# Performance work log

Hardware: AMD Instinct MI355X
Metric: run time of the kernel (lower is better)

Reference implementation:

```python
import jax, jax.numpy as jnp
import numpy as np

LOG_HALF = float(np.log(0.5))  # log_g(0) = log(relu(0)+0.5) = log(0.5)

def log_g(x):
    # log of g(x) = where(x>=0, x+0.5, sigmoid(x))
    return jnp.where(x >= 0.0, jnp.log(jnp.maximum(x, 0.0) + 0.5), -jax.nn.softplus(-x))

def setup_inputs() -> dict:
    key = jax.random.key(0)
    k1, k2, k3, k4 = jax.random.split(key, 4)
    B, T, D, E = 4, 4096, 1024, 1536
    x = jax.random.normal(k1, (B, T, D), dtype=jnp.float32)
    W_f = jax.random.normal(k2, (2 * E, D), dtype=jnp.float32) * 0.02
    b_f = jax.random.normal(k3, (2 * E,), dtype=jnp.float32) * 0.02
    W_down = jax.random.normal(k4, (D, E), dtype=jnp.float32) * 0.02
    return {"x": x, "W_f": W_f, "b_f": b_f, "W_down": W_down}

def reference(x, W_f, b_f, W_down):
    B, T, D = x.shape
    E = W_down.shape[1]
    # fused input projection, split into gate pre-act k and candidate pre-act h_x
    kz, h_x = jnp.split(jnp.einsum('btd,ed->bte', x, W_f) + b_f, 2, axis=-1)
    log_z = -jax.nn.softplus(-kz)          # log sigmoid(k)
    log_coeffs = -jax.nn.softplus(kz)      # log (1 - sigmoid(k))
    log_tilde_h = log_g(h_x)
    # prepend initial log hidden state log_g(0) = log 0.5
    log_h0 = jnp.full((B, 1, E), LOG_HALF, dtype=x.dtype)
    log_values = jnp.concatenate([log_h0, log_tilde_h + log_z], axis=1)  # (B, T+1, E)
    # a_star = pad(cumsum(log_coeffs), one zero row at front along time)
    a_star = jnp.concatenate(
        [jnp.zeros((B, 1, E), dtype=x.dtype), jnp.cumsum(log_coeffs, axis=1)], axis=1)
    log_h = a_star + jax.lax.cumlogsumexp(log_values - a_star, axis=1)
    h = jnp.exp(log_h)[:, 1:]              # (B, T, E)
    return jnp.einsum('bte,de->btd', h, W_down)
```

## Files before the change

### kernel.cpp

```cpp
#include <hip/hip_runtime.h>
#include <hip/hip_bf16.h>
#include <stdint.h>


typedef __bf16 bf16x8 __attribute__((ext_vector_type(8)));
typedef float  f32x4  __attribute__((ext_vector_type(4)));

__device__ __forceinline__ uint16_t f32_to_bf16(float f) {
  union { float f; uint32_t u; } v; v.f = f;
  uint32_t r = (v.u + 0x7FFFu + ((v.u >> 16) & 1u)) >> 16;
  return (uint16_t)r;
}
__device__ __forceinline__ float bf16_to_f32(uint16_t u) {
  union { uint32_t u; float f; } v; v.u = ((uint32_t)u) << 16;
  return v.f;
}

__device__ __forceinline__ void gload_lds16(const uint16_t* g, uint16_t* l) {
  __builtin_amdgcn_global_load_lds(
      (__attribute__((address_space(1))) void*)(g),
      (__attribute__((address_space(3))) void*)(l), 16, 0, 0);
}

__device__ __forceinline__ void gate_val(float kz, float hx, float& a, float& v) {
  float ek = __expf(-fabsf(kz));
  float r  = __builtin_amdgcn_rcpf(1.0f + ek);
  float z  = (kz >= 0.0f) ? r : ek * r;
  a        = (kz >= 0.0f) ? ek * r : r;
  float eh = __expf(fminf(hx, 0.0f));
  float g  = (hx >= 0.0f) ? (hx + 0.5f)
                          : eh * __builtin_amdgcn_rcpf(1.0f + eh);
  v = z * g;
}
__device__ __forceinline__ void gate_from_u32(uint32_t u, float& a, float& v) {
  float kz = bf16_to_f32((uint16_t)(u & 0xFFFFu));
  float hx = bf16_to_f32((uint16_t)(u >> 16));
  gate_val(kz, hx, a, v);
}

__device__ __forceinline__ void cast4(const float* s, uint16_t* d, int j) {
  float4 v = reinterpret_cast<const float4*>(s)[j];
  ushort4 o;
  o.x = f32_to_bf16(v.x); o.y = f32_to_bf16(v.y);
  o.z = f32_to_bf16(v.z); o.w = f32_to_bf16(v.w);
  reinterpret_cast<ushort4*>(d)[j] = o;
}

__global__ __launch_bounds__(256) void cast_all(
    const float* __restrict__ x,   uint16_t* __restrict__ x_bf,
    const float* __restrict__ W_f, uint16_t* __restrict__ Wf_bf,
    const float* __restrict__ b_f, float* __restrict__ bias_p,
    const float* __restrict__ W_d, uint16_t* __restrict__ Wd_bf) {
  const int stride = gridDim.x * blockDim.x;
  const int gid = blockIdx.x * blockDim.x + threadIdx.x;
  if (gid < 3072)
    bias_p[gid] = b_f[(gid & 1) ? 1536 + (gid >> 1) : (gid >> 1)];
  for (int i = gid; i < 4194304; i += stride) cast4(x, x_bf, i);
  for (int i = gid; i < 786432; i += stride) {
    const int r = i >> 8, cg = i & 255;
    const int rp = (r < 1536) ? (r << 1) : (((r - 1536) << 1) | 1);
    float4 v = reinterpret_cast<const float4*>(W_f)[i];
    ushort4 o;
    o.x = f32_to_bf16(v.x); o.y = f32_to_bf16(v.y);
    o.z = f32_to_bf16(v.z); o.w = f32_to_bf16(v.w);
    reinterpret_cast<ushort4*>(Wf_bf)[rp * 256 + cg] = o;
  }
  for (int i = gid; i < 393216; i += stride) cast4(W_d, Wd_bf, i);
}

template <int OUT_BF16_BIAS, int FUSE_SCAN>
__global__ __launch_bounds__(512, 2) void gemm256(
    const uint16_t* __restrict__ A, const uint16_t* __restrict__ Bt,
    const float* __restrict__ bias, void* __restrict__ Cout,
    float* __restrict__ Ac, float* __restrict__ Vc,
    int M, int N, int K) {
  __shared__ alignas(16) uint16_t lds[4 * 16384];

  const int tid  = threadIdx.x;
  const int wave = tid >> 6;
  const int lane = tid & 63;
  const int wr = wave >> 2;
  const int wc = wave & 3;

  const int bid = (int)blockIdx.x;
  const int xq  = bid & 7;
  const int j   = bid >> 3;
  const int pi  = xq + ((j >> 3) << 3);
  const int q   = j & 7;
  const int mt  = ((pi & 31) << 1) + (q >> 2);
  const int nt  = ((pi >> 5) << 2) + (q & 3);
  const int m0  = mt << 8;
  const int n0  = nt << 8;

  const int NT = K >> 5;

  const int srow = wave * 16 + (lane >> 2);
  const int skg  = (lane & 3) ^ ((lane >> 3) & 3);
  const uint16_t* Ag0 = A  + (size_t)(m0 + srow) * K + skg * 8;
  const uint16_t* Ag1 = A  + (size_t)(m0 + 128 + srow) * K + skg * 8;
  const uint16_t* Bg0 = Bt + (size_t)(n0 + srow) * K + skg * 8;
  const uint16_t* Bg1 = Bt + (size_t)(n0 + 128 + srow) * K + skg * 8;
  const int sdw = wave * 512;

  const int kgq = (lane >> 4) ^ ((lane >> 1) & 3);
  const int rA = (wr * 128 + (lane & 15)) * 32 + kgq * 8;
  const int rB = (wc * 64  + (lane & 15)) * 32 + kgq * 8;

  f32x4 acc[8][4] = {};

#pragma unroll
  for (int tt = 0; tt < 3; ++tt) {
    uint16_t* sb = &lds[tt * 16384];
    gload_lds16(Ag0 + tt * 32, sb + sdw);
    gload_lds16(Ag1 + tt * 32, sb + 4096 + sdw);
    gload_lds16(Bg0 + tt * 32, sb + 8192 + sdw);
    gload_lds16(Bg1 + tt * 32, sb + 12288 + sdw);
  }

  for (int u = 0; u < NT; ++u) {
    const uint16_t* Ab = &lds[(u & 3) * 16384 + rA];
    const uint16_t* Bb = &lds[(u & 3) * 16384 + 8192 + rB];
    const int us = (u + 3 < NT) ? (u + 3) : (NT - 1);
    uint16_t* sb = &lds[((u + 3) & 3) * 16384];
    const size_t kofs = (size_t)us * 32;

    asm volatile("s_waitcnt vmcnt(8)" ::: "memory");
    __builtin_amdgcn_s_barrier();

    bf16x8 af0[4], af1[4], bfr[4];
#pragma unroll
    for (int m = 0; m < 4; ++m) af0[m] = *reinterpret_cast<const bf16x8*>(Ab + m * 512);
#pragma unroll
    for (int n = 0; n < 4; ++n) bfr[n] = *reinterpret_cast<const bf16x8*>(Bb + n * 512);
    gload_lds16(Ag0 + kofs, sb + sdw);
    gload_lds16(Ag1 + kofs, sb + 4096 + sdw);
    __builtin_amdgcn_sched_barrier(0);
    __builtin_amdgcn_s_barrier();
    asm volatile("s_waitcnt lgkmcnt(0)" ::: "memory");
    __builtin_amdgcn_sched_barrier(0);
    __builtin_amdgcn_s_setprio(1);
#pragma unroll
    for (int m = 0; m < 4; ++m)
#pragma unroll
      for (int n = 0; n < 4; ++n)
        acc[m][n] = __builtin_amdgcn_mfma_f32_16x16x32_bf16(bfr[n], af0[m], acc[m][n], 0, 0, 0);
    __builtin_amdgcn_s_setprio(0);
    __builtin_amdgcn_sched_barrier(0);

#pragma unroll
    for (int m = 0; m < 4; ++m) af1[m] = *reinterpret_cast<const bf16x8*>(Ab + (m + 4) * 512);
    gload_lds16(Bg0 + kofs, sb + 8192 + sdw);
    gload_lds16(Bg1 + kofs, sb + 12288 + sdw);
    __builtin_amdgcn_sched_barrier(0);
    __builtin_amdgcn_s_barrier();
    asm volatile("s_waitcnt lgkmcnt(0)" ::: "memory");
    __builtin_amdgcn_sched_barrier(0);
    __builtin_amdgcn_s_setprio(1);
#pragma unroll
    for (int m = 0; m < 4; ++m)
#pragma unroll
      for (int n = 0; n < 4; ++n)
        acc[m + 4][n] = __builtin_amdgcn_mfma_f32_16x16x32_bf16(bfr[n], af1[m], acc[m + 4][n], 0, 0, 0);
    __builtin_amdgcn_s_setprio(0);
    __builtin_amdgcn_sched_barrier(0);
  }
  asm volatile("s_waitcnt vmcnt(0)" ::: "memory");

  const int r0 = m0 + wr * 128 + (lane & 15);
  const int cb = n0 + wc * 64 + (lane >> 4) * 4;
  if constexpr (OUT_BF16_BIAS) {
    uint16_t* C = (uint16_t*)Cout;
    if constexpr (FUSE_SCAN) {
      __builtin_amdgcn_s_barrier();
    }
    char* lb = (char*)lds;
    float bv[4][4];
#pragma unroll
    for (int n = 0; n < 4; ++n) {
      const float4 b4 = *reinterpret_cast<const float4*>(&bias[cb + n * 16]);
      bv[n][0] = b4.x; bv[n][1] = b4.y; bv[n][2] = b4.z; bv[n][3] = b4.w;
    }
#pragma unroll
    for (int m = 0; m < 8; ++m) {
      const int row = r0 + m * 16;
#pragma unroll
      for (int n = 0; n < 4; ++n) {
        const int col = cb + n * 16;
        ushort4 o;
        o.x = f32_to_bf16(acc[m][n][0] + bv[n][0]);
        o.y = f32_to_bf16(acc[m][n][1] + bv[n][1]);
        o.z = f32_to_bf16(acc[m][n][2] + bv[n][2]);
        o.w = f32_to_bf16(acc[m][n][3] + bv[n][3]);
        *reinterpret_cast<ushort4*>(&C[(size_t)row * N + col]) = o;
        if constexpr (FUSE_SCAN) {
          const int lr   = wr * 128 + m * 16 + (lane & 15);
          const int slot = wc * 16 + n * 4 + (lane >> 4);
          const int boff = lr * 512 + ((slot * 8) ^ ((lr & 15) << 3));
          uint2 pr;
          pr.x = (uint32_t)o.x | ((uint32_t)o.y << 16);
          pr.y = (uint32_t)o.z | ((uint32_t)o.w << 16);
          *reinterpret_cast<uint2*>(lb + boff) = pr;
        }
      }
    }

    if constexpr (FUSE_SCAN) {
      asm volatile("s_waitcnt lgkmcnt(0)" ::: "memory");
      __builtin_amdgcn_s_barrier();
      const int cidx = tid >> 7;
      const int eloc = tid & 127;
      float Aa = 1.0f, Vv = 0.0f;
#pragma unroll 8
      for (int t = 0; t < 64; ++t) {
        const int lr   = cidx * 64 + t;
        const int boff = lr * 512 + ((((eloc >> 1) * 8) ^ ((lr & 15) << 3)) +
                                     (eloc & 1) * 4);
        uint32_t u32 = *reinterpret_cast<const uint32_t*>(lb + boff);
        float a, v; gate_from_u32(u32, a, v);
        Aa *= a;
        Vv = a * Vv + v;
      }
      const int b  = m0 >> 12;
      const int c  = ((m0 & 4095) >> 6) + cidx;
      const int E2 = N >> 1;
      const size_t idx = ((size_t)(b * 64 + c)) * E2 + (n0 >> 1) + eloc;
      Ac[idx] = Aa; Vc[idx] = Vv;
    }
  } else {
    float* C = (float*)Cout;
#pragma unroll
    for (int m = 0; m < 8; ++m) {
      const int row = r0 + m * 16;
#pragma unroll
      for (int n = 0; n < 4; ++n) {
        const int col = cb + n * 16;
        float4 o;
        o.x = acc[m][n][0]; o.y = acc[m][n][1];
        o.z = acc[m][n][2]; o.w = acc[m][n][3];
        *reinterpret_cast<float4*>(&C[(size_t)row * N + col]) = o;
      }
    }
  }
}

__global__ __launch_bounds__(256) void scan_pass3(
    const uint16_t* __restrict__ proj, const float* __restrict__ Ac,
    const float* __restrict__ Vc, uint16_t* __restrict__ hout,
    int T, int E, int CH, int L) {
  const int e = blockIdx.x * 256 + threadIdx.x;
  const int c = blockIdx.y;
  const int b = blockIdx.z;
  const int N1 = 2 * E;
  float h = 0.5f;
  for (int cc = 0; cc < c; ++cc) {
    const size_t idx = ((size_t)(b * CH + cc)) * E + e;
    h = Ac[idx] * h + Vc[idx];
  }
  const uint16_t* p = proj + (size_t)(b * T + c * L) * N1 + 2 * e;
  uint16_t* o = hout + (size_t)(b * T + c * L) * E + e;
#pragma unroll 4
  for (int t = 0; t < L; ++t) {
    float a, v; gate_from_u32(*reinterpret_cast<const uint32_t*>(p), a, v);
    h = a * h + v;
    *o = f32_to_bf16(h);
    p += N1; o += E;
  }
}

extern "C" void kernel_launch(void* const* d_in, const int* in_sizes, int n_in,
                              void* d_out, int out_size, void* d_ws, size_t ws_size,
                              hipStream_t stream) {
  const float* x   = (const float*)d_in[0];
  const float* W_f = (const float*)d_in[1];
  const float* b_f = (const float*)d_in[2];
  const float* W_d = (const float*)d_in[3];
  const int Bb = 4, T = 4096, D = 1024, E = 1536;
  const int M = Bb * T;
  const int N1 = 2 * E;
  const int CH = 64, L = T / CH;

  char* w = (char*)d_ws;
  uint16_t* x_bf  = (uint16_t*)w; w += (size_t)M * D * 2;
  uint16_t* Wf_bf = (uint16_t*)w; w += (size_t)N1 * D * 2;
  uint16_t* Wd_bf = (uint16_t*)w; w += (size_t)D * E * 2;
  uint16_t* proj  = (uint16_t*)w; w += (size_t)M * N1 * 2;
  uint16_t* h_bf  = (uint16_t*)w; w += (size_t)M * E * 2;
  float* Ac     = (float*)w; w += (size_t)Bb * CH * E * 4;
  float* Vc     = (float*)w; w += (size_t)Bb * CH * E * 4;
  float* bias_p = (float*)w; w += (size_t)N1 * 4;

  cast_all<<<2048, 256, 0, stream>>>(x, x_bf, W_f, Wf_bf, b_f, bias_p, W_d, Wd_bf);

  gemm256<1, 1><<<(M / 256) * (N1 / 256), 512, 0, stream>>>(
      x_bf, Wf_bf, bias_p, proj, Ac, Vc, M, N1, D);

  scan_pass3<<<dim3(E / 256, CH, Bb), 256, 0, stream>>>(proj, Ac, Vc, h_bf, T, E, CH, L);

  gemm256<0, 0><<<(M / 256) * (D / 256), 512, 0, stream>>>(
      h_bf, Wd_bf, nullptr, d_out, nullptr, nullptr, M, D, E);
}
```

Before: 236.9 us.

## Switch GEMM mainloop to double-buffered K=64 tiles with 8-way LDS swizzle

The GEMM mainloop changes from a 4-stage ring of K=32 tiles to 2 buffers of K=64 tiles. Each iteration now runs four MFMA phases, and the XOR swizzle over 8 k-groups is redone for 128-byte rows. This halves the number of loop iterations and waits per unit of K, which should cut barrier and waitcnt overhead. The cost is a shallower prefetch: it waits with vmcnt(0), so global-load latency is hidden less, and stalls may become exposed.

```diff
diff --git a/kernel.cpp b/kernel.cpp
--- a/kernel.cpp
+++ b/kernel.cpp
@@ -74,7 +74,7 @@
     const float* __restrict__ bias, void* __restrict__ Cout,
     float* __restrict__ Ac, float* __restrict__ Vc,
     int M, int N, int K) {
-  __shared__ alignas(16) uint16_t lds[4 * 16384];
+  __shared__ alignas(16) uint16_t lds[2 * 32768];
 
   const int tid  = threadIdx.x;
   const int wave = tid >> 6;
@@ -92,48 +92,51 @@
   const int m0  = mt << 8;
   const int n0  = nt << 8;
 
-  const int NT = K >> 5;
-
-  const int srow = wave * 16 + (lane >> 2);
-  const int skg  = (lane & 3) ^ ((lane >> 3) & 3);
-  const uint16_t* Ag0 = A  + (size_t)(m0 + srow) * K + skg * 8;
-  const uint16_t* Ag1 = A  + (size_t)(m0 + 128 + srow) * K + skg * 8;
-  const uint16_t* Bg0 = Bt + (size_t)(n0 + srow) * K + skg * 8;
-  const uint16_t* Bg1 = Bt + (size_t)(n0 + 128 + srow) * K + skg * 8;
+  const int NT2 = K >> 6;
+
+  const int srow8 = wave * 8 + (lane >> 3);
+  const int skg   = (lane & 7) ^ ((lane >> 3) & 7);
+  const uint16_t* Ag[4];
+  const uint16_t* Bg[4];
+#pragma unroll
+  for (int r = 0; r < 4; ++r) {
+    Ag[r] = A  + (size_t)(m0 + r * 64 + srow8) * K + skg * 8;
+    Bg[r] = Bt + (size_t)(n0 + r * 64 + srow8) * K + skg * 8;
+  }
   const int sdw = wave * 512;
 
-  const int kgq = (lane >> 4) ^ ((lane >> 1) & 3);
-  const int rA = (wr * 128 + (lane & 15)) * 32 + kgq * 8;
-  const int rB = (wc * 64  + (lane & 15)) * 32 + kgq * 8;
+  const int rowA = (wr * 128 + (lane & 15)) * 64;
+  const int rowB = (wc * 64  + (lane & 15)) * 64;
+  const int sl0  = ((lane >> 4) ^ (lane & 7)) << 3;
+  const int sl1  = (((lane >> 4) ^ 4) ^ (lane & 7)) << 3;
+  const int rA0 = rowA + sl0, rA1 = rowA + sl1;
+  const int rB0 = rowB + sl0, rB1 = rowB + sl1;
 
   f32x4 acc[8][4] = {};
 
 #pragma unroll
-  for (int tt = 0; tt < 3; ++tt) {
-    uint16_t* sb = &lds[tt * 16384];
-    gload_lds16(Ag0 + tt * 32, sb + sdw);
-    gload_lds16(Ag1 + tt * 32, sb + 4096 + sdw);
-    gload_lds16(Bg0 + tt * 32, sb + 8192 + sdw);
-    gload_lds16(Bg1 + tt * 32, sb + 12288 + sdw);
-  }
-
-  for (int u = 0; u < NT; ++u) {
-    const uint16_t* Ab = &lds[(u & 3) * 16384 + rA];
-    const uint16_t* Bb = &lds[(u & 3) * 16384 + 8192 + rB];
-    const int us = (u + 3 < NT) ? (u + 3) : (NT - 1);
-    uint16_t* sb = &lds[((u + 3) & 3) * 16384];
-    const size_t kofs = (size_t)us * 32;
-
-    asm volatile("s_waitcnt vmcnt(8)" ::: "memory");
+  for (int r = 0; r < 4; ++r) {
+    gload_lds16(Ag[r], &lds[r * 4096 + sdw]);
+    gload_lds16(Bg[r], &lds[16384 + r * 4096 + sdw]);
+  }
+
+  for (int u = 0; u < NT2; ++u) {
+    const uint16_t* Ab = &lds[(u & 1) * 32768];
+    const uint16_t* Bb = Ab + 16384;
+    const int ts = (u + 1 < NT2) ? (u + 1) : (NT2 - 1);
+    uint16_t* sb = &lds[((u + 1) & 1) * 32768];
+    const size_t kofs = (size_t)ts * 64;
+
+    asm volatile("s_waitcnt vmcnt(0)" ::: "memory");
     __builtin_amdgcn_s_barrier();
 
     bf16x8 af0[4], af1[4], bfr[4];
 #pragma unroll
-    for (int m = 0; m < 4; ++m) af0[m] = *reinterpret_cast<const bf16x8*>(Ab + m * 512);
-#pragma unroll
-    for (int n = 0; n < 4; ++n) bfr[n] = *reinterpret_cast<const bf16x8*>(Bb + n * 512);
-    gload_lds16(Ag0 + kofs, sb + sdw);
-    gload_lds16(Ag1 + kofs, sb + 4096 + sdw);
+    for (int m = 0; m < 4; ++m) af0[m] = *reinterpret_cast<const bf16x8*>(Ab + rA0 + m * 1024);
+#pragma unroll
+    for (int n = 0; n < 4; ++n) bfr[n] = *reinterpret_cast<const bf16x8*>(Bb + rB0 + n * 1024);
+#pragma unroll
+    for (int r = 0; r < 4; ++r) gload_lds16(Ag[r] + kofs, sb + r * 4096 + sdw);
     __builtin_amdgcn_sched_barrier(0);
     __builtin_amdgcn_s_barrier();
     asm volatile("s_waitcnt lgkmcnt(0)" ::: "memory");
@@ -148,9 +151,41 @@
     __builtin_amdgcn_sched_barrier(0);
 
 #pragma unroll
-    for (int m = 0; m < 4; ++m) af1[m] = *reinterpret_cast<const bf16x8*>(Ab + (m + 4) * 512);
-    gload_lds16(Bg0 + kofs, sb + 8192 + sdw);
-    gload_lds16(Bg1 + kofs, sb + 12288 + sdw);
+    for (int m = 0; m < 4; ++m) af1[m] = *reinterpret_cast<const bf16x8*>(Ab + rA0 + (m + 4) * 1024);
+#pragma unroll
+    for (int r = 0; r < 4; ++r) gload_lds16(Bg[r] + kofs, sb + 16384 + r * 4096 + sdw);
+    __builtin_amdgcn_sched_barrier(0);
+    __builtin_amdgcn_s_barrier();
+    asm volatile("s_waitcnt lgkmcnt(0)" ::: "memory");
+    __builtin_amdgcn_sched_barrier(0);
+    __builtin_amdgcn_s_setprio(1);
+#pragma unroll
+    for (int m = 0; m < 4; ++m)
+#pragma unroll
+      for (int n = 0; n < 4; ++n)
+        acc[m + 4][n] = __builtin_amdgcn_mfma_f32_16x16x32_bf16(bfr[n], af1[m], acc[m + 4][n], 0, 0, 0);
+    __builtin_amdgcn_s_setprio(0);
+    __builtin_amdgcn_sched_barrier(0);
+
+#pragma unroll
+    for (int m = 0; m < 4; ++m) af0[m] = *reinterpret_cast<const bf16x8*>(Ab + rA1 + m * 1024);
+#pragma unroll
+    for (int n = 0; n < 4; ++n) bfr[n] = *reinterpret_cast<const bf16x8*>(Bb + rB1 + n * 1024);
+    __builtin_amdgcn_sched_barrier(0);
+    __builtin_amdgcn_s_barrier();
+    asm volatile("s_waitcnt lgkmcnt(0)" ::: "memory");
+    __builtin_amdgcn_sched_barrier(0);
+    __builtin_amdgcn_s_setprio(1);
+#pragma unroll
+    for (int m = 0; m < 4; ++m)
+#pragma unroll
+      for (int n = 0; n < 4; ++n)
+        acc[m][n] = __builtin_amdgcn_mfma_f32_16x16x32_bf16(bfr[n], af0[m], acc[m][n], 0, 0, 0);
+    __builtin_amdgcn_s_setprio(0);
+    __builtin_amdgcn_sched_barrier(0);
+
+#pragma unroll
+    for (int m = 0; m < 4; ++m) af1[m] = *reinterpret_cast<const bf16x8*>(Ab + rA1 + (m + 4) * 1024);
     __builtin_amdgcn_sched_barrier(0);
     __builtin_amdgcn_s_barrier();
     asm volatile("s_waitcnt lgkmcnt(0)" ::: "memory");
```

Measured after the change: 233.5 us. No clear change (-1.4%).
